# Kernel tuning notes

Measured on AMD Instinct MI355X. Metric: run time of the kernel, lower is better.

## Reference

```python
import jax, jax.numpy as jnp
import numpy as np

N, F, E, WID, M, K = 100000, 128, 128, 4, 25000, 16
HID = WID * F    # width * num_features = 512
DHID = WID * E   # discriminator hidden = 512
EPS = 1e-5


def _v2v(x, v_idx, w_e):
    """Hypergraph v2v mean aggregation: v->e mean (scaled by w_e), then e->v mean."""
    Mm, Kk = v_idx.shape
    C = x.shape[1]
    ef = jnp.zeros((Mm, C), x.dtype)
    for k in range(Kk):  # K is small and static; avoids a [M,K,C] materialization
        ef = ef + x[v_idx[:, k]]
    ef = ef * (w_e / Kk)[:, None]  # weighted edge features [M, C]
    out = jnp.zeros_like(x)
    deg = jnp.zeros((x.shape[0],), x.dtype)
    for k in range(Kk):
        out = out.at[v_idx[:, k]].add(ef)
        deg = deg.at[v_idx[:, k]].add(1.0)
    return out / jnp.maximum(deg, 1.0)[:, None]


def _bn(h, g, bt):
    # BatchNorm1d in training mode: biased batch stats over vertex dim
    m = h.mean(0)
    v = ((h - m) ** 2).mean(0)
    return g * (h - m) * jax.lax.rsqrt(v + EPS) + bt


def _conv(x, Wt, b, g, bt, v_idx, w_e, last=False):
    h = _bn(x @ Wt.T + b, g, bt)
    h = _v2v(h, v_idx, w_e)
    return h if last else jax.nn.relu(h)  # dropout = identity (eval mode)


def setup_inputs() -> dict:
    key = jax.random.key(0)
    ks = iter(jax.random.split(key, 64))

    def lin(o, i):
        s = 1.0 / np.sqrt(i)
        return (jax.random.uniform(next(ks), (o, i), minval=-s, maxval=s, dtype=jnp.float32),
                jax.random.uniform(next(ks), (o,), minval=-s, maxval=s, dtype=jnp.float32))

    d = {}
    d["X"] = jax.random.normal(next(ks), (N, F), dtype=jnp.float32)
    d["v_idx"] = jax.random.randint(next(ks), (M, K), 0, N, dtype=jnp.int32)
    d["w_e"] = jax.random.uniform(next(ks), (M,), dtype=jnp.float32)
    for name, (o, i) in [("enc1", (HID, F)), ("enc2", (E, HID)), ("fc", (E, HID)),
                         ("f1u", (E, E)), ("f2u", (E, E)), ("f1r", (E, E)), ("f2r", (E, E)),
                         ("f1", (E, E)), ("f2", (E, E)),
                         ("dis1", (DHID, E)), ("dis2", (2, DHID)),
                         ("dec1", (HID, E)), ("dec2", (F, HID))]:
        Wt, b = lin(o, i)
        d[name + "_W"] = Wt
        d[name + "_b"] = b
    for name, c in [("enc1", HID), ("enc2", E), ("dis1", DHID), ("dis2", 2), ("dec1", HID), ("dec2", F)]:
        d[name + "_g"] = jnp.ones((c,), jnp.float32)
        d[name + "_bt"] = jnp.zeros((c,), jnp.float32)
    return d


def reference(X, v_idx, w_e,
              enc1_W, enc1_b, enc2_W, enc2_b, fc_W, fc_b,
              f1u_W, f1u_b, f2u_W, f2u_b, f1r_W, f1r_b, f2r_W, f2r_b,
              f1_W, f1_b, f2_W, f2_b,
              dis1_W, dis1_b, dis2_W, dis2_b, dec1_W, dec1_b, dec2_W, dec2_b,
              enc1_g, enc1_bt, enc2_g, enc2_bt, dis1_g, dis1_bt, dis2_g, dis2_bt,
              dec1_g, dec1_bt, dec2_g, dec2_bt):
    # encoder (returns last output and first-layer output)
    x1 = _conv(X, enc1_W, enc1_b, enc1_g, enc1_bt, v_idx, w_e)            # [N, HID]
    xe = _conv(x1, enc2_W, enc2_b, enc2_g, enc2_bt, v_idx, w_e, last=True)  # [N, E]
    xe1 = x1 @ fc_W.T + fc_b                                               # [N, E]
    # GRU-style gating
    z = jax.nn.sigmoid(xe1 @ f1u_W.T + f1u_b + xe @ f2u_W.T + f2u_b)
    r = jax.nn.sigmoid(xe1 @ f1r_W.T + f1r_b + xe @ f2r_W.T + f2r_b)
    o = jnp.tanh(xe1 @ f1_W.T + f1_b + (r * xe) @ f2_W.T + f2_b)
    outs = z * o + (1.0 - z) * xe                                          # [N, E]
    # attention pooling (n = input_size - 1)
    dd = (outs - outs.mean(0)) ** 2
    vv = dd.sum(0) / (N - 1)
    ee = dd / (4.0 * (vv + 0.001)) + 0.5
    proto = (outs * jax.nn.sigmoid(ee)).sum(0)                             # [E]
    # gradient reversal is identity in the forward pass
    h = _conv(outs, dis1_W, dis1_b, dis1_g, dis1_bt, v_idx, w_e)
    xdis = _conv(h, dis2_W, dis2_b, dis2_g, dis2_bt, v_idx, w_e, last=True)  # [N, 2]
    h = _conv(outs, dec1_W, dec1_b, dec1_g, dec1_bt, v_idx, w_e)
    x_de = _conv(h, dec2_W, dec2_b, dec2_g, dec2_bt, v_idx, w_e, last=True)  # [N, F]
    return (outs, x_de, proto, xdis)
```

## Files before the change

kernel.cpp:

```cpp
#include <hip/hip_runtime.h>
#include <cstddef>
#include <cstdint>

static constexpr int NV = 100000;
static constexpr int NP = 100096;
static constexpr int ME = 25000;
static constexpr int MEP = 25088;
static constexpr int KE = 16;
static constexpr float BN_EPS = 1e-5f;

typedef unsigned int u32;
typedef __attribute__((ext_vector_type(8))) short s16x8;
typedef __attribute__((ext_vector_type(8))) unsigned short u16x8;
typedef __attribute__((ext_vector_type(4))) float f32x4;

__device__ __forceinline__ float sigm(float x) { return 1.0f / (1.0f + expf(-x)); }
__device__ __forceinline__ float bf2f(unsigned short u) {
    union { u32 i; float f; } v; v.i = ((u32)u) << 16; return v.f;
}
__device__ __forceinline__ unsigned short f2bf(float f) {
    union { float f; u32 i; } v; v.f = f;
    u32 u = v.i;
    return (unsigned short)((u + 0x7FFFu + ((u >> 16) & 1u)) >> 16);
}

#define GLD16(g, l) __builtin_amdgcn_global_load_lds(                          \
    (__attribute__((address_space(1))) const unsigned int*)(g),                \
    (__attribute__((address_space(3))) unsigned int*)(l), 16, 0, 0)

#define STAGE_AB(b, k0)                                                        \
  {                                                                            \
    unsigned short* sA_ = sm + (b) * 12288;                                    \
    unsigned short* sB_ = sA_ + 8192;                                          \
    _Pragma("unroll")                                                          \
    for (int i_ = 0; i_ < 4; ++i_) {                                           \
      const unsigned short* g_ = A + (size_t)(bm + 32 * w + 8 * i_ + (l >> 3)) * IC + (k0) + swz; \
      GLD16(g_, sA_ + 2048 * w + 512 * i_);                                    \
    }                                                                          \
    _Pragma("unroll")                                                          \
    for (int i_ = 0; i_ < 2; ++i_) {                                           \
      const unsigned short* g_ = W + (size_t)(bn + 16 * w + 8 * i_ + (l >> 3)) * IC + (k0) + swz; \
      GLD16(g_, sB_ + 1024 * w + 512 * i_);                                    \
    }                                                                          \
  }

__global__ __launch_bounds__(256)
void mfma_gemm(const unsigned short* __restrict__ A, int IC,
               const unsigned short* __restrict__ W, const float* __restrict__ bias,
               unsigned short* __restrict__ Cb, int ldb, int cb0,
               unsigned short* __restrict__ Cb2, int ldb2, int splitN,
               float* __restrict__ s1f, float* __restrict__ s2f, int statsC)
{
    __shared__ unsigned short sm[2 * 12288];
    const int bm = blockIdx.y * 128;
    const int bn = blockIdx.x * 64;
    const int tid = threadIdx.x;
    const int l = tid & 63, w = tid >> 6;
    const int wrow = w >> 1, wcol = w & 1;

    f32x4 acc[4][2];
    #pragma unroll
    for (int m = 0; m < 4; ++m)
        #pragma unroll
        for (int n = 0; n < 2; ++n)
            #pragma unroll
            for (int r = 0; r < 4; ++r) acc[m][n][r] = 0.f;

    const int swz = (((l & 7) ^ (l >> 3)) << 3);
    const int nt = IC >> 6;

    STAGE_AB(0, 0);
    asm volatile("s_waitcnt vmcnt(0)" ::: "memory");
    __builtin_amdgcn_s_barrier();

    for (int t = 0; t < nt; ++t) {
        const int cur = t & 1;
        if (t + 1 < nt) STAGE_AB(cur ^ 1, (t + 1) << 6);
        const unsigned short* sA = sm + cur * 12288;
        const unsigned short* sB = sA + 8192;
        #pragma unroll
        for (int ks = 0; ks < 2; ++ks) {
            const int koff = ks * 32 + ((l >> 4) << 3);
            s16x8 afr[4], bfr[2];
            #pragma unroll
            for (int m = 0; m < 4; ++m) {
                int row = wrow * 64 + m * 16 + (l & 15);
                afr[m] = *(const s16x8*)&sA[row * 64 + (koff ^ ((l & 7) << 3))];
            }
            #pragma unroll
            for (int n = 0; n < 2; ++n) {
                int col = wcol * 32 + n * 16 + (l & 15);
                bfr[n] = *(const s16x8*)&sB[col * 64 + (koff ^ ((l & 7) << 3))];
            }
            #pragma unroll
            for (int m = 0; m < 4; ++m)
                #pragma unroll
                for (int n = 0; n < 2; ++n)
                    acc[m][n] = __builtin_amdgcn_mfma_f32_16x16x32_bf16(
                        afr[m], bfr[n], acc[m][n], 0, 0, 0);
        }
        asm volatile("s_waitcnt vmcnt(0)" ::: "memory");
        __builtin_amdgcn_s_barrier();
    }

    unsigned short* dst = Cb;
    int ld = ldb, co = cb0;
    if (Cb2 && bn >= splitN) { dst = Cb2; ld = ldb2; co = -splitN; }

    #pragma unroll
    for (int n = 0; n < 2; ++n) {
        const int col = bn + wcol * 32 + n * 16 + (l & 15);
        const float bs = bias[col];
        float ssum = 0.f, sq = 0.f;
        #pragma unroll
        for (int m = 0; m < 4; ++m) {
            const int row0 = bm + wrow * 64 + m * 16 + ((l >> 4) << 2);
            #pragma unroll
            for (int r = 0; r < 4; ++r) {
                float v = acc[m][n][r] + bs;
                int row = row0 + r;
                if (dst) dst[(size_t)row * ld + co + col] = f2bf(v);
                if (s1f && col < statsC && row < NV) { ssum += v; sq += v * v; }
            }
        }
        if (s1f && col < statsC) {
            ssum += __shfl_xor(ssum, 16); ssum += __shfl_xor(ssum, 32);
            sq   += __shfl_xor(sq, 16);   sq   += __shfl_xor(sq, 32);
            if ((l >> 4) == 0) {
                atomicAdd(&s1f[col], ssum);
                atomicAdd(&s2f[col], sq);
            }
        }
    }
}

__global__ __launch_bounds__(256)
void mfma_gemm_ef(const unsigned short* __restrict__ A,
                  const unsigned short* __restrict__ W,
                  const float* __restrict__ we,
                  const float* __restrict__ P, const float* __restrict__ Q,
                  unsigned short* __restrict__ ef, int ldE)
{
    const int IC = 128;
    __shared__ unsigned short sm[2 * 12288];
    const int bm = blockIdx.y * 128;
    const int bn = blockIdx.x * 64;
    const int tid = threadIdx.x;
    const int l = tid & 63, w = tid >> 6;
    const int wrow = w >> 1, wcol = w & 1;

    f32x4 acc[4][2];
    #pragma unroll
    for (int m = 0; m < 4; ++m)
        #pragma unroll
        for (int n = 0; n < 2; ++n)
            #pragma unroll
            for (int r = 0; r < 4; ++r) acc[m][n][r] = 0.f;

    const int swz = (((l & 7) ^ (l >> 3)) << 3);

    STAGE_AB(0, 0);
    asm volatile("s_waitcnt vmcnt(0)" ::: "memory");
    __builtin_amdgcn_s_barrier();

    #pragma unroll
    for (int t = 0; t < 2; ++t) {
        const int cur = t & 1;
        if (t == 0) STAGE_AB(1, 64);
        const unsigned short* sA = sm + cur * 12288;
        const unsigned short* sB = sA + 8192;
        #pragma unroll
        for (int ks = 0; ks < 2; ++ks) {
            const int koff = ks * 32 + ((l >> 4) << 3);
            s16x8 afr[4], bfr[2];
            #pragma unroll
            for (int m = 0; m < 4; ++m) {
                int row = wrow * 64 + m * 16 + (l & 15);
                afr[m] = *(const s16x8*)&sA[row * 64 + (koff ^ ((l & 7) << 3))];
            }
            #pragma unroll
            for (int n = 0; n < 2; ++n) {
                int col = wcol * 32 + n * 16 + (l & 15);
                bfr[n] = *(const s16x8*)&sB[col * 64 + (koff ^ ((l & 7) << 3))];
            }
            #pragma unroll
            for (int m = 0; m < 4; ++m)
                #pragma unroll
                for (int n = 0; n < 2; ++n)
                    acc[m][n] = __builtin_amdgcn_mfma_f32_16x16x32_bf16(
                        afr[m], bfr[n], acc[m][n], 0, 0, 0);
        }
        asm volatile("s_waitcnt vmcnt(0)" ::: "memory");
        __builtin_amdgcn_s_barrier();
    }

    #pragma unroll
    for (int n = 0; n < 2; ++n) {
        const int col = bn + wcol * 32 + n * 16 + (l & 15);
        const float pc = P[col], qc = Q[col];
        #pragma unroll
        for (int m = 0; m < 4; ++m) {
            const int row0 = bm + wrow * 64 + m * 16 + ((l >> 4) << 2);
            #pragma unroll
            for (int r = 0; r < 4; ++r) {
                int row = row0 + r;
                if (row < ME) {
                    float wv = we[row];
                    ef[(size_t)row * ldE + col] = f2bf(wv * (pc * acc[m][n][r] + qc));
                }
            }
        }
    }
}

__global__ __launch_bounds__(256)
void cov_kernel(const unsigned short* __restrict__ A, float* __restrict__ cov)
{
    __shared__ unsigned short T[128 * 64];
    const int tid = threadIdx.x;
    const int l = tid & 63, w = tid >> 6;

    f32x4 acc[2][8];
    #pragma unroll
    for (int m = 0; m < 2; ++m)
        #pragma unroll
        for (int n = 0; n < 8; ++n)
            #pragma unroll
            for (int r = 0; r < 4; ++r) acc[m][n][r] = 0.f;

    const int r0 = blockIdx.x * 1024;
    for (int ch = 0; ch < 16; ++ch) {
        const int rbase = r0 + ch * 64;
        __syncthreads();
        #pragma unroll
        for (int q = 0; q < 4; ++q) {
            int idx = tid + q * 256;
            int r = idx & 63, cg = idx >> 6;
            int row = rbase + r;
            u16x8 u = {0, 0, 0, 0, 0, 0, 0, 0};
            if (row < NV) u = *(const u16x8*)&A[(size_t)row * 128 + cg * 8];
            #pragma unroll
            for (int j = 0; j < 8; ++j) {
                int c = cg * 8 + j;
                T[c * 64 + (r ^ ((c & 7) << 3))] = u[j];
            }
        }
        __syncthreads();
        #pragma unroll
        for (int ks = 0; ks < 2; ++ks) {
            const int koff = ks * 32 + ((l >> 4) << 3);
            s16x8 fi[2], fj[8];
            #pragma unroll
            for (int m = 0; m < 2; ++m) {
                int c = (w * 2 + m) * 16 + (l & 15);
                fi[m] = *(const s16x8*)&T[c * 64 + (koff ^ ((c & 7) << 3))];
            }
            #pragma unroll
            for (int n = 0; n < 8; ++n) {
                int c = n * 16 + (l & 15);
                fj[n] = *(const s16x8*)&T[c * 64 + (koff ^ ((c & 7) << 3))];
            }
// ... 84 lines not shown
    } else if (i < 492800) {
        int o = i - 492544;
        bzr[o] = (o < 128) ? (f1ub[o] + f2ub[o]) : (f1rb[o - 128] + f2rb[o - 128]);
    } else if (i < 492928) {
        int o = i - 492800;
        bo[o] = f1b[o] + f2b[o];
    } else if (i < 493952) {
        int o = i - 492928;
        bdd[o] = (o < 512) ? ds1b[o] : dc1b[o - 512];
    } else if (i < 494208) {
        int o = i - 493952;
        bef[o] = (o < 128) ? e2b[o] : fcb[o - 128];
    }
}

__global__ void cvt_f32_bf16(const float* __restrict__ in, unsigned short* __restrict__ out, int n)
{
    int i = (blockIdx.x * 256 + threadIdx.x) * 4;
    if (i < n) {
        float4 v = *reinterpret_cast<const float4*>(&in[i]);
        out[i] = f2bf(v.x); out[i + 1] = f2bf(v.y);
        out[i + 2] = f2bf(v.z); out[i + 3] = f2bf(v.w);
    }
}

__global__ void bn_finalize_kernel(const float* __restrict__ s1, const float* __restrict__ s2,
                                   const float* __restrict__ g, const float* __restrict__ bt,
                                   float* __restrict__ scale, float* __restrict__ shift,
                                   int C, float invN)
{
    int c = threadIdx.x;
    if (c < C) {
        float m = s1[c] * invN;
        float v = fmaxf(s2[c] * invN - m * m, 0.f);
        float sc = g[c] * rsqrtf(v + BN_EPS);
        scale[c] = sc;
        shift[c] = bt[c] - m * sc;
    }
}

__global__ void bn_finalize_pq(const float* __restrict__ s1, const float* __restrict__ s2,
                               const float* __restrict__ g, const float* __restrict__ bt,
                               const float* __restrict__ bias,
                               float* __restrict__ P, float* __restrict__ Q,
                               int C, int off, float invN)
{
    int c = threadIdx.x;
    if (c < C) {
        int cc = off + c;
        float m = s1[cc] * invN;
        float v = fmaxf(s2[cc] * invN - m * m, 0.f);
        float sc = g[c] * rsqrtf(v + BN_EPS);
        float sh = bt[c] - m * sc;
        P[cc] = sc * (1.0f / KE);
        Q[cc] = sc * bias[c] + sh;
    }
}

__global__ __launch_bounds__(256)
void edge_gather_sum(const unsigned short* __restrict__ x, const int* __restrict__ vidx,
                     unsigned short* __restrict__ ge)
{
    const int e = blockIdx.x * 16 + (threadIdx.x >> 4);
    const int cp = (threadIdx.x & 15) << 3;
    if (e >= ME) return;
    float s[8] = {};
    const int* vi = vidx + e * KE;
    #pragma unroll
    for (int k = 0; k < KE; ++k) {
        int v = vi[k];
        u16x8 u = *(const u16x8*)&x[(size_t)v * 128 + cp];
        #pragma unroll
        for (int j = 0; j < 8; ++j) s[j] += bf2f(u[j]);
    }
    u16x8 o;
    #pragma unroll
    for (int j = 0; j < 8; ++j) o[j] = f2bf(s[j]);
    *(u16x8*)&ge[(size_t)e * 128 + cp] = o;
}

__global__ __launch_bounds__(256)
void edge_gather_bf(const unsigned short* __restrict__ pre, const int* __restrict__ vidx,
                    const float* __restrict__ we, const float* __restrict__ scl,
                    const float* __restrict__ shf, unsigned short* __restrict__ ef, int C)
{
    const int tpe = C >> 3;
    const int epb = 256 / tpe;
    const int e = blockIdx.x * epb + threadIdx.x / tpe;
    const int cp = (threadIdx.x % tpe) << 3;
    if (e >= ME) return;
    float s[8] = {};
    const int* vi = vidx + e * KE;
    #pragma unroll
    for (int k = 0; k < KE; ++k) {
        int v = vi[k];
        u16x8 u = *(const u16x8*)&pre[(size_t)v * C + cp];
        #pragma unroll
        for (int j = 0; j < 8; ++j) s[j] += bf2f(u[j]);
    }
    float wv = we[e] * (1.0f / KE);
    u16x8 o;
    #pragma unroll
    for (int j = 0; j < 8; ++j)
        o[j] = f2bf(wv * (scl[cp + j] * s[j] + (float)KE * shf[cp + j]));
    *(u16x8*)&ef[(size_t)e * C + cp] = o;
}

__global__ void edge_gather2_kernel(const float* __restrict__ X, const int* __restrict__ vidx,
                                    const float* __restrict__ we, const float* __restrict__ scale,
                                    const float* __restrict__ shift, float* __restrict__ ef)
{
    int e = blockIdx.x * blockDim.x + threadIdx.x;
    if (e >= ME) return;
    float s0 = 0.f, s1v = 0.f;
    #pragma unroll
    for (int k = 0; k < KE; ++k) {
        int v = vidx[e * KE + k];
        s0 += X[2 * v];
        s1v += X[2 * v + 1];
    }
    float w = we[e] * (1.0f / KE);
    ef[2 * e]     = w * (scale[0] * s0 + (float)KE * shift[0]);
    ef[2 * e + 1] = w * (scale[1] * s1v + (float)KE * shift[1]);
}

__global__ void deg_kernel(const int* __restrict__ vidx, int* __restrict__ deg)
{
    int i = blockIdx.x * blockDim.x + threadIdx.x;
    if (i < ME * KE) atomicAdd(&deg[vidx[i]], 1);
}

// ... 51 lines not shown

__global__ __launch_bounds__(256)
void csr_gather_bf(const unsigned short* __restrict__ ef, int ldE, int cb0E,
                   const int* __restrict__ rowptr, const int* __restrict__ csr,
                   float* __restrict__ outf, int ldf,
                   unsigned short* __restrict__ outb, int ldb, int cb0,
                   unsigned short* __restrict__ outb2, int ldb2,
                   int C, int relu)
{
    const int lpv = C >> 3;
    const int vpb = 256 / lpv;
    const int v = blockIdx.x * vpb + threadIdx.x / lpv;
    const int lg = threadIdx.x % lpv;
    if (v >= NV) return;
    const int s = rowptr[v], e = rowptr[v + 1];
    float a[8] = {};
    int i = s;
    for (; i + 2 <= e; i += 2) {
        int e0 = csr[i], e1 = csr[i + 1];
        u16x8 u0 = *(const u16x8*)&ef[(size_t)e0 * ldE + cb0E + lg * 8];
        u16x8 u1 = *(const u16x8*)&ef[(size_t)e1 * ldE + cb0E + lg * 8];
        #pragma unroll
        for (int j = 0; j < 8; ++j) a[j] += bf2f(u0[j]) + bf2f(u1[j]);
    }
    if (i < e) {
        int e0 = csr[i];
        u16x8 u0 = *(const u16x8*)&ef[(size_t)e0 * ldE + cb0E + lg * 8];
        #pragma unroll
        for (int j = 0; j < 8; ++j) a[j] += bf2f(u0[j]);
    }
    float inv = 1.0f / (float)max(e - s, 1);
    #pragma unroll
    for (int j = 0; j < 8; ++j) {
        float x = a[j] * inv;
        if (relu) x = fmaxf(x, 0.f);
        a[j] = x;
    }
    if (outf) {
        float* p = outf + (size_t)v * ldf + lg * 8;
        #pragma unroll
        for (int j = 0; j < 8; ++j) p[j] = a[j];
    }
    if (outb) {
        u16x8 o;
        #pragma unroll
        for (int j = 0; j < 8; ++j) o[j] = f2bf(a[j]);
        *(u16x8*)&outb[(size_t)v * ldb + cb0 + lg * 8] = o;
    }
    if (outb2) {
        u16x8 o;
        #pragma unroll
        for (int j = 0; j < 8; ++j) o[j] = f2bf(a[j]);
        *(u16x8*)&outb2[(size_t)v * ldb2 + lg * 8] = o;
    }
}

__global__ __launch_bounds__(256)
void csr_gather_dd(const unsigned short* __restrict__ ef,
                   const int* __restrict__ rowptr, const int* __restrict__ csr,
                   const unsigned short* __restrict__ wdis2, const float* __restrict__ dis2b,
                   float* __restrict__ pre22, unsigned short* __restrict__ hdec)
{
    const int w = threadIdx.x >> 6, l = threadIdx.x & 63;
    const int v = blockIdx.x * 2 + (w >> 1);
    const int half = w & 1;
    const int s = rowptr[v], e = rowptr[v + 1];
    const int cp = half * 512 + l * 8;
    float a[8] = {};
    int i = s;
    for (; i + 2 <= e; i += 2) {
        int e0 = csr[i], e1 = csr[i + 1];
        u16x8 u0 = *(const u16x8*)&ef[(size_t)e0 * 1024 + cp];
        u16x8 u1 = *(const u16x8*)&ef[(size_t)e1 * 1024 + cp];
        #pragma unroll
        for (int j = 0; j < 8; ++j) a[j] += bf2f(u0[j]) + bf2f(u1[j]);
    }
    if (i < e) {
        int e0 = csr[i];
        u16x8 u0 = *(const u16x8*)&ef[(size_t)e0 * 1024 + cp];
        #pragma unroll
        for (int j = 0; j < 8; ++j) a[j] += bf2f(u0[j]);
    }
    float inv = 1.0f / (float)max(e - s, 1);
    #pragma unroll
    for (int j = 0; j < 8; ++j) a[j] = fmaxf(a[j] * inv, 0.f);
    if (half == 0) {
        u16x8 w0 = *(const u16x8*)&wdis2[l * 8];
        u16x8 w1 = *(const u16x8*)&wdis2[512 + l * 8];
        float d0 = 0.f, d1 = 0.f;
        #pragma unroll
        for (int j = 0; j < 8; ++j) {
            d0 += a[j] * bf2f(w0[j]);
            d1 += a[j] * bf2f(w1[j]);
        }
        for (int o = 32; o > 0; o >>= 1) {
            d0 += __shfl_down(d0, o);
            d1 += __shfl_down(d1, o);
        }
        if (l == 0) {
            pre22[2 * v]     = d0 + dis2b[0];
            pre22[2 * v + 1] = d1 + dis2b[1];
        }
    } else {
        u16x8 o8;
        #pragma unroll
        for (int j = 0; j < 8; ++j) o8[j] = f2bf(a[j]);
        *(u16x8*)&hdec[(size_t)v * 512 + l * 8] = o8;
    }
}

__global__ void csr_gather2_kernel(const float* __restrict__ ef, const int* __restrict__ rowptr,
                                   const int* __restrict__ csr, float* __restrict__ outp)
{
    int v = blockIdx.x * blockDim.x + threadIdx.x;
    if (v >= NV) return;
    int s = rowptr[v], e = rowptr[v + 1];
    float a0 = 0.f, a1 = 0.f;
    for (int i = s; i < e; ++i) {
        int ed = csr[i];
        a0 += ef[2 * ed];
        a1 += ef[2 * ed + 1];
    }
    float inv = 1.0f / (float)max(e - s, 1);
    outp[2 * v]     = a0 * inv;
    outp[2 * v + 1] = a1 * inv;
}

__global__ __launch_bounds__(256)
void colstats_bf(const unsigned short* __restrict__ Xb,
                 float* __restrict__ s1, float* __restrict__ s2)
{
    const int t = threadIdx.x;
    const int cg = t & 15;
    const int rs = t >> 4;
    float s[8] = {}, q[8] = {};
    for (int r = blockIdx.x * 16 + rs; r < NV; r += 256 * 16) {
        u16x8 u = *(const u16x8*)&Xb[(size_t)r * 128 + cg * 8];
        #pragma unroll
        for (int j = 0; j < 8; ++j) {
            float v = bf2f(u[j]);
            s[j] += v; q[j] += v * v;
        }
    }
    __shared__ float ls[16][16][8];
    __shared__ float lq[16][16][8];
    #pragma unroll
    for (int j = 0; j < 8; ++j) { ls[rs][cg][j] = s[j]; lq[rs][cg][j] = q[j]; }
    __syncthreads();
    int c = t & 127;
    float a = 0.f;
    if (t < 128) {
        #pragma unroll
        for (int i = 0; i < 16; ++i) a += ls[i][c >> 3][c & 7];
        atomicAdd(&s1[c], a);
    } else {
        #pragma unroll
        for (int i = 0; i < 16; ++i) a += lq[i][c >> 3][c & 7];
        atomicAdd(&s2[c], a);
    }
}
// ... 130 lines not shown
    const float* f1u_W  = (const float*)d_in[9];  const float* f1u_b  = (const float*)d_in[10];
    const float* f2u_W  = (const float*)d_in[11]; const float* f2u_b  = (const float*)d_in[12];
    const float* f1r_W  = (const float*)d_in[13]; const float* f1r_b  = (const float*)d_in[14];
    const float* f2r_W  = (const float*)d_in[15]; const float* f2r_b  = (const float*)d_in[16];
    const float* f1_W   = (const float*)d_in[17]; const float* f1_b   = (const float*)d_in[18];
    const float* f2_W   = (const float*)d_in[19]; const float* f2_b   = (const float*)d_in[20];
    const float* dis1_W = (const float*)d_in[21]; const float* dis1_b = (const float*)d_in[22];
    const float* dis2_W = (const float*)d_in[23]; const float* dis2_b = (const float*)d_in[24];
    const float* dec1_W = (const float*)d_in[25]; const float* dec1_b = (const float*)d_in[26];
    const float* dec2_W = (const float*)d_in[27]; const float* dec2_b = (const float*)d_in[28];
    const float* enc1_g = (const float*)d_in[29]; const float* enc1_bt = (const float*)d_in[30];
    const float* enc2_g = (const float*)d_in[31]; const float* enc2_bt = (const float*)d_in[32];
    const float* dis1_g = (const float*)d_in[33]; const float* dis1_bt = (const float*)d_in[34];
    const float* dis2_g = (const float*)d_in[35]; const float* dis2_bt = (const float*)d_in[36];
    const float* dec1_g = (const float*)d_in[37]; const float* dec1_bt = (const float*)d_in[38];
    const float* dec2_g = (const float*)d_in[39]; const float* dec2_bt = (const float*)d_in[40];

    float* out   = (float*)d_out;
    float* outs  = out;
    float* x_de  = out + 12800000;
    float* proto = out + 25600000;
    float* xdis  = out + 25600128;

    char* base = (char*)d_ws;
    unsigned short* bufA = (unsigned short*)base;
    char* p = base + (size_t)NP * 512 * 2;
    unsigned short* bufE = (unsigned short*)p; p += (size_t)MEP * 1024 * 2;
    unsigned short* Greg = (unsigned short*)p;
    unsigned short* Xbf  = Greg;
    unsigned short* outsb = Greg + (size_t)NP * 128;
    p += (size_t)NP * 256 * 2;
    unsigned short* x1bf = (unsigned short*)p; p += (size_t)NP * 512 * 2;
    unsigned short* WB = (unsigned short*)p; p += 492544 * 2 + 1024;
    float* bzr = (float*)p; p += 256 * 4;
    float* bo  = (float*)p; p += 128 * 4;
    float* bdd = (float*)p; p += 1024 * 4;
    float* bef = (float*)p; p += 256 * 4;
    float* s1  = (float*)p; p += 1024 * 4;
    float* s2  = (float*)p; p += 1024 * 4;
    float* scl = (float*)p; p += 1024 * 4;
    float* shf = (float*)p; p += 1024 * 4;
    float* sX1 = (float*)p; p += 128 * 4;
    float* sX2 = (float*)p; p += 128 * 4;
    float* sA1 = (float*)p; p += 128 * 4;
    float* sA2 = (float*)p; p += 128 * 4;
    float* covX = (float*)p; p += 16384 * 4;
    float* covA = (float*)p; p += 16384 * 4;
    int* deg    = (int*)p; p += (size_t)NV * 4;
    int* rowptr = (int*)p; p += (size_t)(NV + 1) * 4;
    int* cursor = (int*)p; p += (size_t)NV * 4;
    int* bsums  = (int*)p; p += 512 * 4;
    int* csr    = (int*)p; p += (size_t)ME * KE * 4;
    float* outsf = (float*)p; p += (size_t)NP * 128 * 4;
    unsigned short* ge = (unsigned short*)p;

    unsigned short* pre128 = bufA;
    unsigned short* xe_bf  = bufA + (size_t)NP * 128;
    unsigned short* ZR     = bufA + (size_t)NP * 256;
    unsigned short* Opre   = bufA;
    unsigned short* hdec   = bufA;
    float* pre22 = (float*)(Greg + (size_t)NP * 128);
    float* bufEf = (float*)bufE;

    unsigned short* wenc1 = WB;
    unsigned short* wenc2 = WB + 65536;
    unsigned short* wdd   = WB + 196608;
    unsigned short* wdec2 = WB + 327680;
    unsigned short* wdis2 = WB + 393216;
    unsigned short* wzr   = WB + 394240;
    unsigned short* wo    = WB + 459776;

    const int n128 = NV * 128;
    const int n8 = n128 / 8;
    const int nScanBlocks = (NV + 255) / 256;

    auto gemm = [&](const unsigned short* A, int ic, const unsigned short* W, const float* b,
                    unsigned short* Cb, int ldb, int cb0,
                    unsigned short* Cb2, int ldb2, int splitN,
                    int oc, float* st1, float* st2, int statsC) {
        dim3 g(oc / 64, NP / 128);
        mfma_gemm<<<g, 256, 0, stream>>>(A, ic, W, b, Cb, ldb, cb0, Cb2, ldb2, splitN,
                                         st1, st2, statsC);
    };

    prep_weights<<<1931, 256, 0, stream>>>(enc1_W, enc2_W, fc_W, dis1_W, dec1_W, dec2_W, dis2_W,
                                           f1u_W, f2u_W, f1r_W, f2r_W, f1_W, f2_W,
                                           f1u_b, f2u_b, f1r_b, f2r_b, f1_b, f2_b,
                                           dis1_b, dec1_b, enc2_b, fc_b,
                                           WB, bzr, bo, bdd, bef);
    cvt_f32_bf16<<<(n128 / 4 + 255) / 256, 256, 0, stream>>>(X, Xbf, n128);

    hipMemsetAsync(deg, 0, NV * sizeof(int), stream);
    deg_kernel<<<(ME * KE + 255) / 256, 256, 0, stream>>>(vidx, deg);
    scan_block_kernel<<<nScanBlocks, 256, 0, stream>>>(deg, rowptr, bsums, NV);
    scan_sums_par<<<1, 512, 0, stream>>>(bsums, nScanBlocks);
    scan_add_kernel<<<nScanBlocks, 256, 0, stream>>>(rowptr, bsums, NV);
    hipMemcpyAsync(cursor, rowptr, NV * sizeof(int), hipMemcpyDeviceToDevice, stream);
    csr_fill_kernel<<<(ME * KE + 255) / 256, 256, 0, stream>>>(vidx, cursor, csr);

    hipMemsetAsync(sX1, 0, 256 * sizeof(float), stream);
    hipMemsetAsync(covX, 0, 16384 * sizeof(float), stream);
    colstats_bf<<<256, 256, 0, stream>>>(Xbf, sX1, sX2);
    cov_kernel<<<98, 256, 0, stream>>>(Xbf, covX);
    quadform_kernel<<<512, 128, 0, stream>>>(covX, sX1, wenc1, enc1_b, s1, s2);
    bn_finalize_pq<<<1, 512, 0, stream>>>(s1, s2, enc1_g, enc1_bt, enc1_b, scl, shf, 512, 0, 1.0f / NV);
    edge_gather_sum<<<(ME + 15) / 16, 256, 0, stream>>>(Xbf, vidx, ge);
    { dim3 g(8, MEP / 128);
      mfma_gemm_ef<<<g, 256, 0, stream>>>(ge, wenc1, we, scl, shf, bufE, 512); }
    csr_gather_bf<<<NV / 4, 256, 0, stream>>>(bufE, 512, 0, rowptr, csr,
        nullptr, 0, x1bf, 512, 0, nullptr, 0, 512, 1);

    hipMemsetAsync(s1, 0, 2048 * sizeof(float), stream);
    gemm(x1bf, 512, wenc2, bef, pre128, 128, 0, Greg, 256, 128, 256, s1, s2, 128);
    bn_finalize_kernel<<<1, 512, 0, stream>>>(s1, s2, enc2_g, enc2_bt, scl, shf, 128, 1.0f / NV);
    edge_gather_bf<<<(ME + 15) / 16, 256, 0, stream>>>(pre128, vidx, we, scl, shf, bufE, 128);
    csr_gather_bf<<<NV / 16, 256, 0, stream>>>(bufE, 128, 0, rowptr, csr,
        nullptr, 0, Greg, 256, 128, xe_bf, 128, 128, 0);

    gemm(Greg, 256, wzr, bzr, ZR, 256, 0, nullptr, 0, 1 << 30, 256, nullptr, nullptr, 0);
    rx_kernel<<<(n8 + 255) / 256, 256, 0, stream>>>(ZR, xe_bf, Greg, n8);
    gemm(Greg, 256, wo, bo, Opre, 128, 0, nullptr, 0, 1 << 30, 128, nullptr, nullptr, 0);
    gru_out_kernel<<<(n8 + 255) / 256, 256, 0, stream>>>(ZR, Opre, xe_bf, outs, outsb, outsf, n8);

    hipMemsetAsync(sA1, 0, 256 * sizeof(float), stream);
    colstats_bf<<<256, 256, 0, stream>>>(outsb, sA1, sA2);
    att_finalize_kernel<<<1, 128, 0, stream>>>(sA1, sA2, scl, shf, 128);
    hipMemsetAsync(proto, 0, 128 * sizeof(float), stream);
    proto_ws<<<256, 256, 0, stream>>>(outsf, scl, shf, proto);

    hipMemsetAsync(covA, 0, 16384 * sizeof(float), stream);
    cov_kernel<<<98, 256, 0, stream>>>(outsb, covA);
    quadform_kernel<<<1024, 128, 0, stream>>>(covA, sA1, wdd, bdd, s1, s2);
    bn_finalize_pq<<<1, 512, 0, stream>>>(s1, s2, dis1_g, dis1_bt, dis1_b, scl, shf, 512, 0, 1.0f / NV);
    bn_finalize_pq<<<1, 512, 0, stream>>>(s1, s2, dec1_g, dec1_bt, dec1_b, scl, shf, 512, 512, 1.0f / NV);
    edge_gather_sum<<<(ME + 15) / 16, 256, 0, stream>>>(outsb, vidx, ge);
    { dim3 g(16, MEP / 128);
      mfma_gemm_ef<<<g, 256, 0, stream>>>(ge, wdd, we, scl, shf, bufE, 1024); }
    csr_gather_dd<<<NV / 2, 256, 0, stream>>>(bufE, rowptr, csr, wdis2, dis2_b, pre22, hdec);

    hipMemsetAsync(s1, 0, 2048 * sizeof(float), stream);
    colstats2_kernel<<<64, 256, 0, stream>>>(pre22, NV, s1, s2);
    bn_finalize_kernel<<<1, 512, 0, stream>>>(s1, s2, dis2_g, dis2_bt, scl, shf, 2, 1.0f / NV);
    edge_gather2_kernel<<<(ME + 255) / 256, 256, 0, stream>>>(pre22, vidx, we, scl, shf, bufEf);
    csr_gather2_kernel<<<(NV + 255) / 256, 256, 0, stream>>>(bufEf, rowptr, csr, xdis);

    hipMemsetAsync(s1, 0, 2048 * sizeof(float), stream);
    gemm(hdec, 512, wdec2, dec2_b, Greg, 128, 0, nullptr, 0, 1 << 30, 128, s1, s2, 128);
    bn_finalize_kernel<<<1, 512, 0, stream>>>(s1, s2, dec2_g, dec2_bt, scl, shf, 128, 1.0f / NV);
    edge_gather_bf<<<(ME + 15) / 16, 256, 0, stream>>>(Greg, vidx, we, scl, shf, bufE, 128);
    csr_gather_bf<<<NV / 16, 256, 0, stream>>>(bufE, 128, 0, rowptr, csr,
        x_de, 128, nullptr, 0, 0, nullptr, 0, 128, 0);
}
```

Measured before the change: 901.1 us.

## Reorder v2v aggregation before the linear layer to gather narrow inputs

Uses linearity of BN-affine plus mean aggregation to move the weighted edge-to-vertex gather onto the 128-wide input features. Each vertex gets a weighted sum of incident edge sums and a mean edge weight, and the 512/1024-wide GEMM then runs on the vertex rows with ReLU and the BN scale/shift applied in its epilogue. This removes the wide per-edge output buffer and the wide CSR gather over it. The dis2 projection is folded into the GEMM epilogue through shuffle reductions and atomics into pre22. In exchange the GEMM covers four times as many rows, bf16 rounding happens at a different point, and the dis2 bias is dropped because the following batch norm cancels it.

```diff
diff --git a/kernel.cpp b/kernel.cpp
--- a/kernel.cpp
+++ b/kernel.cpp
@@ -135,11 +135,13 @@
 }
 
 __global__ __launch_bounds__(256)
-void mfma_gemm_ef(const unsigned short* __restrict__ A,
-                  const unsigned short* __restrict__ W,
-                  const float* __restrict__ we,
-                  const float* __restrict__ P, const float* __restrict__ Q,
-                  unsigned short* __restrict__ ef, int ldE)
+void mfma_gemm_vtx(const unsigned short* __restrict__ A,
+                   const unsigned short* __restrict__ W,
+                   const float* __restrict__ P, const float* __restrict__ Q,
+                   const float* __restrict__ sw,
+                   unsigned short* __restrict__ dst, int ldd, int colStart,
+                   const unsigned short* __restrict__ disW,
+                   float* __restrict__ pre22)
 {
     const int IC = 128;
     __shared__ unsigned short sm[2 * 12288];
@@ -194,19 +196,44 @@
         __builtin_amdgcn_s_barrier();
     }
 
-    #pragma unroll
-    for (int n = 0; n < 2; ++n) {
-        const int col = bn + wcol * 32 + n * 16 + (l & 15);
-        const float pc = P[col], qc = Q[col];
+    if (disW && bn < colStart) {
         #pragma unroll
         for (int m = 0; m < 4; ++m) {
-            const int row0 = bm + wrow * 64 + m * 16 + ((l >> 4) << 2);
             #pragma unroll
             for (int r = 0; r < 4; ++r) {
-                int row = row0 + r;
-                if (row < ME) {
-                    float wv = we[row];
-                    ef[(size_t)row * ldE + col] = f2bf(wv * (pc * acc[m][n][r] + qc));
+                const int row = bm + wrow * 64 + m * 16 + ((l >> 4) << 2) + r;
+                const float swr = sw[row];
+                float p0 = 0.f, p1 = 0.f;
+                #pragma unroll
+                for (int n = 0; n < 2; ++n) {
+                    const int col = bn + wcol * 32 + n * 16 + (l & 15);
+                    float h = fmaxf(P[col] * acc[m][n][r] + swr * Q[col], 0.f);
+                    p0 += h * bf2f(disW[col]);
+                    p1 += h * bf2f(disW[512 + col]);
+                }
+                p0 += __shfl_xor(p0, 1); p0 += __shfl_xor(p0, 2);
+                p0 += __shfl_xor(p0, 4); p0 += __shfl_xor(p0, 8);
+                p1 += __shfl_xor(p1, 1); p1 += __shfl_xor(p1, 2);
+                p1 += __shfl_xor(p1, 4); p1 += __shfl_xor(p1, 8);
+                if ((l & 15) == 0 && row < NV) {
+                    atomicAdd(&pre22[2 * row], p0);
+                    atomicAdd(&pre22[2 * row + 1], p1);
+                }
+            }
+        }
+    } else {
+        #pragma unroll
+        for (int n = 0; n < 2; ++n) {
+            const int col = bn + wcol * 32 + n * 16 + (l & 15);
+            const float pc = P[col], qc = Q[col];
+            #pragma unroll
+            for (int m = 0; m < 4; ++m) {
+                const int row0 = bm + wrow * 64 + m * 16 + ((l >> 4) << 2);
+                #pragma unroll
+                for (int r = 0; r < 4; ++r) {
+                    const int row = row0 + r;
+                    float h = fmaxf(pc * acc[m][n][r] + sw[row] * qc, 0.f);
+                    dst[(size_t)row * ldd + col - colStart] = f2bf(h);
                 }
             }
         }
@@ -397,7 +424,7 @@
         float v = fmaxf(s2[cc] * invN - m * m, 0.f);
         float sc = g[c] * rsqrtf(v + BN_EPS);
         float sh = bt[c] - m * sc;
-        P[cc] = sc * (1.0f / KE);
+        P[cc] = sc;
         Q[cc] = sc * bias[c] + sh;
     }
 }
@@ -422,6 +449,40 @@
     #pragma unroll
     for (int j = 0; j < 8; ++j) o[j] = f2bf(s[j]);
     *(u16x8*)&ge[(size_t)e * 128 + cp] = o;
+}
+
+__global__ __launch_bounds__(256)
+void csr_gather_g2(const unsigned short* __restrict__ ge, const float* __restrict__ we,
+                   const int* __restrict__ rowptr, const int* __restrict__ csr,
+                   unsigned short* __restrict__ g2, float* __restrict__ swv)
+{
+    const int v = blockIdx.x * 16 + (threadIdx.x >> 4);
+    const int lg = threadIdx.x & 15;
+    if (v >= NP) return;
+    if (v >= NV) {
+        u16x8 z = {0, 0, 0, 0, 0, 0, 0, 0};
+        *(u16x8*)&g2[(size_t)v * 128 + lg * 8] = z;
+        if (swv && lg == 0) swv[v] = 0.f;
+        return;
+    }
+    const int s = rowptr[v], e = rowptr[v + 1];
+    float a[8] = {};
+    float ws = 0.f;
+    for (int i = s; i < e; ++i) {
+        int ed = csr[i];
+        float wt = we[ed];
+        ws += wt;
+        u16x8 u = *(const u16x8*)&ge[(size_t)ed * 128 + lg * 8];
+        #pragma unroll
+        for (int j = 0; j < 8; ++j) a[j] = fmaf(wt, bf2f(u[j]), a[j]);
+    }
+    float inv = 1.0f / (float)max(e - s, 1);
+    float invK = inv * (1.0f / KE);
+    u16x8 o;
+    #pragma unroll
+    for (int j = 0; j < 8; ++j) o[j] = f2bf(a[j] * invK);
+    *(u16x8*)&g2[(size_t)v * 128 + lg * 8] = o;
+    if (swv && lg == 0) swv[v] = ws * inv;
 }
 
 __global__ __launch_bounds__(256)
@@ -579,60 +640,6 @@
         #pragma unroll
         for (int j = 0; j < 8; ++j) o[j] = f2bf(a[j]);
         *(u16x8*)&outb2[(size_t)v * ldb2 + lg * 8] = o;
-    }
-}
-
-__global__ __launch_bounds__(256)
-void csr_gather_dd(const unsigned short* __restrict__ ef,
-                   const int* __restrict__ rowptr, const int* __restrict__ csr,
-                   const unsigned short* __restrict__ wdis2, const float* __restrict__ dis2b,
-                   float* __restrict__ pre22, unsigned short* __restrict__ hdec)
-{
-    const int w = threadIdx.x >> 6, l = threadIdx.x & 63;
-    const int v = blockIdx.x * 2 + (w >> 1);
-    const int half = w & 1;
-    const int s = rowptr[v], e = rowptr[v + 1];
-    const int cp = half * 512 + l * 8;
-    float a[8] = {};
-    int i = s;
-    for (; i + 2 <= e; i += 2) {
-        int e0 = csr[i], e1 = csr[i + 1];
-        u16x8 u0 = *(const u16x8*)&ef[(size_t)e0 * 1024 + cp];
-        u16x8 u1 = *(const u16x8*)&ef[(size_t)e1 * 1024 + cp];
-        #pragma unroll
-        for (int j = 0; j < 8; ++j) a[j] += bf2f(u0[j]) + bf2f(u1[j]);
-    }
-    if (i < e) {
-        int e0 = csr[i];
-        u16x8 u0 = *(const u16x8*)&ef[(size_t)e0 * 1024 + cp];
-        #pragma unroll
-        for (int j = 0; j < 8; ++j) a[j] += bf2f(u0[j]);
-    }
-    float inv = 1.0f / (float)max(e - s, 1);
-    #pragma unroll
-    for (int j = 0; j < 8; ++j) a[j] = fmaxf(a[j] * inv, 0.f);
-    if (half == 0) {
-        u16x8 w0 = *(const u16x8*)&wdis2[l * 8];
-        u16x8 w1 = *(const u16x8*)&wdis2[512 + l * 8];
-        float d0 = 0.f, d1 = 0.f;
-        #pragma unroll
-        for (int j = 0; j < 8; ++j) {
-            d0 += a[j] * bf2f(w0[j]);
-            d1 += a[j] * bf2f(w1[j]);
-        }
-        for (int o = 32; o > 0; o >>= 1) {
-            d0 += __shfl_down(d0, o);
-            d1 += __shfl_down(d1, o);
-        }
-        if (l == 0) {
-            pre22[2 * v]     = d0 + dis2b[0];
-            pre22[2 * v + 1] = d1 + dis2b[1];
-        }
-    } else {
-        u16x8 o8;
-        #pragma unroll
-        for (int j = 0; j < 8; ++j) o8[j] = f2bf(a[j]);
-        *(u16x8*)&hdec[(size_t)v * 512 + l * 8] = o8;
     }
 }
 
@@ -869,7 +876,10 @@
     int* bsums  = (int*)p; p += 512 * 4;
     int* csr    = (int*)p; p += (size_t)ME * KE * 4;
     float* outsf = (float*)p; p += (size_t)NP * 128 * 4;
-    unsigned short* ge = (unsigned short*)p;
+    unsigned short* ge = (unsigned short*)p; p += (size_t)MEP * 128 * 2;
+    float* sw = (float*)p;
+
+    unsigned short* g2 = bufE + (size_t)MEP * 128;
 
     unsigned short* pre128 = bufA;
     unsigned short* xe_bf  = bufA + (size_t)NP * 128;
@@ -922,10 +932,10 @@
     quadform_kernel<<<512, 128, 0, stream>>>(covX, sX1, wenc1, enc1_b, s1, s2);
     bn_finalize_pq<<<1, 512, 0, stream>>>(s1, s2, enc1_g, enc1_bt, enc1_b, scl, shf, 512, 0, 1.0f / NV);
     edge_gather_sum<<<(ME + 15) / 16, 256, 0, stream>>>(Xbf, vidx, ge);
-    { dim3 g(8, MEP / 128);
-      mfma_gemm_ef<<<g, 256, 0, stream>>>(ge, wenc1, we, scl, shf, bufE, 512); }
-    csr_gather_bf<<<NV / 4, 256, 0, stream>>>(bufE, 512, 0, rowptr, csr,
-        nullptr, 0, x1bf, 512, 0, nullptr, 0, 512, 1);
+    csr_gather_g2<<<NP / 16, 256, 0, stream>>>(ge, we, rowptr, csr, g2, sw);
+    { dim3 g(8, NP / 128);
+      mfma_gemm_vtx<<<g, 256, 0, stream>>>(g2, wenc1, scl, shf, sw, x1bf, 512, 0,
+                                           nullptr, nullptr); }
 
     hipMemsetAsync(s1, 0, 2048 * sizeof(float), stream);
     gemm(x1bf, 512, wenc2, bef, pre128, 128, 0, Greg, 256, 128, 256, s1, s2, 128);
@@ -951,9 +961,11 @@
     bn_finalize_pq<<<1, 512, 0, stream>>>(s1, s2, dis1_g, dis1_bt, dis1_b, scl, shf, 512, 0, 1.0f / NV);
     bn_finalize_pq<<<1, 512, 0, stream>>>(s1, s2, dec1_g, dec1_bt, dec1_b, scl, shf, 512, 512, 1.0f / NV);
     edge_gather_sum<<<(ME + 15) / 16, 256, 0, stream>>>(outsb, vidx, ge);
-    { dim3 g(16, MEP / 128);
-      mfma_gemm_ef<<<g, 256, 0, stream>>>(ge, wdd, we, scl, shf, bufE, 1024); }
-    csr_gather_dd<<<NV / 2, 256, 0, stream>>>(bufE, rowptr, csr, wdis2, dis2_b, pre22, hdec);
+    csr_gather_g2<<<NP / 16, 256, 0, stream>>>(ge, we, rowptr, csr, g2, nullptr);
+    hipMemsetAsync(pre22, 0, (size_t)NV * 2 * sizeof(float), stream);
+    { dim3 g(16, NP / 128);
+      mfma_gemm_vtx<<<g, 256, 0, stream>>>(g2, wdd, scl, shf, sw, hdec, 512, 512,
+                                           wdis2, pre22); }
 
     hipMemsetAsync(s1, 0, 2048 * sizeof(float), stream);
     colstats2_kernel<<<64, 256, 0, stream>>>(pre22, NV, s1, s2);
```

After: 938.8 us. +4.2%, slower.

## Read GEMM B operand directly from global and split dis/dec edge buffers

Applied to the files above, without the earlier changes.

The GEMM kernels stop staging the weight (B) tile in shared memory and load B fragments straight from global memory, which cuts LDS use per block and may raise occupancy. This relies on the small weight matrix hitting in cache but adds uncoalesced global loads inside the MFMA loop. The edge-feature GEMM now writes the dis and dec halves into two separate 512-wide buffers. The fused 1024-wide csr gather is replaced by a dis-only gather kernel plus the generic bf16 gather for the dec half. Each gather reads contiguous 512-wide rows, at the cost of an extra launch and a second traversal of the CSR.

```diff
diff --git a/kernel.cpp b/kernel.cpp
--- a/kernel.cpp
+++ b/kernel.cpp
@@ -28,19 +28,13 @@
     (__attribute__((address_space(1))) const unsigned int*)(g),                \
     (__attribute__((address_space(3))) unsigned int*)(l), 16, 0, 0)
 
-#define STAGE_AB(b, k0)                                                        \
+#define STAGE_A(b, k0)                                                         \
   {                                                                            \
-    unsigned short* sA_ = sm + (b) * 12288;                                    \
-    unsigned short* sB_ = sA_ + 8192;                                          \
+    unsigned short* sA_ = sm + (b) * 8192;                                     \
     _Pragma("unroll")                                                          \
     for (int i_ = 0; i_ < 4; ++i_) {                                           \
       const unsigned short* g_ = A + (size_t)(bm + 32 * w + 8 * i_ + (l >> 3)) * IC + (k0) + swz; \
       GLD16(g_, sA_ + 2048 * w + 512 * i_);                                    \
-    }                                                                          \
-    _Pragma("unroll")                                                          \
-    for (int i_ = 0; i_ < 2; ++i_) {                                           \
-      const unsigned short* g_ = W + (size_t)(bn + 16 * w + 8 * i_ + (l >> 3)) * IC + (k0) + swz; \
-      GLD16(g_, sB_ + 1024 * w + 512 * i_);                                    \
     }                                                                          \
   }
 
@@ -51,7 +45,7 @@
                unsigned short* __restrict__ Cb2, int ldb2, int splitN,
                float* __restrict__ s1f, float* __restrict__ s2f, int statsC)
 {
-    __shared__ unsigned short sm[2 * 12288];
+    __shared__ unsigned short sm[2 * 8192];
     const int bm = blockIdx.y * 128;
     const int bn = blockIdx.x * 64;
     const int tid = threadIdx.x;
@@ -69,15 +63,14 @@
     const int swz = (((l & 7) ^ (l >> 3)) << 3);
     const int nt = IC >> 6;
 
-    STAGE_AB(0, 0);
+    STAGE_A(0, 0);
     asm volatile("s_waitcnt vmcnt(0)" ::: "memory");
     __builtin_amdgcn_s_barrier();
 
     for (int t = 0; t < nt; ++t) {
         const int cur = t & 1;
-        if (t + 1 < nt) STAGE_AB(cur ^ 1, (t + 1) << 6);
-        const unsigned short* sA = sm + cur * 12288;
-        const unsigned short* sB = sA + 8192;
+        if (t + 1 < nt) STAGE_A(cur ^ 1, (t + 1) << 6);
+        const unsigned short* sA = sm + cur * 8192;
         #pragma unroll
         for (int ks = 0; ks < 2; ++ks) {
             const int koff = ks * 32 + ((l >> 4) << 3);
@@ -89,8 +82,8 @@
             }
             #pragma unroll
             for (int n = 0; n < 2; ++n) {
-                int col = wcol * 32 + n * 16 + (l & 15);
-                bfr[n] = *(const s16x8*)&sB[col * 64 + (koff ^ ((l & 7) << 3))];
+                int col = bn + wcol * 32 + n * 16 + (l & 15);
+                bfr[n] = *(const s16x8*)&W[(size_t)col * IC + (t << 6) + koff];
             }
             #pragma unroll
             for (int m = 0; m < 4; ++m)
@@ -135,14 +128,14 @@
 }
 
 __global__ __launch_bounds__(256)
-void mfma_gemm_ef(const unsigned short* __restrict__ A,
-                  const unsigned short* __restrict__ W,
-                  const float* __restrict__ we,
-                  const float* __restrict__ P, const float* __restrict__ Q,
-                  unsigned short* __restrict__ ef, int ldE)
+void mfma_gemm_ef2(const unsigned short* __restrict__ A,
+                   const unsigned short* __restrict__ W,
+                   const float* __restrict__ we,
+                   const float* __restrict__ P, const float* __restrict__ Q,
+                   unsigned short* __restrict__ ef0, unsigned short* __restrict__ ef1)
 {
     const int IC = 128;
-    __shared__ unsigned short sm[2 * 12288];
+    __shared__ unsigned short sm[2 * 8192];
     const int bm = blockIdx.y * 128;
     const int bn = blockIdx.x * 64;
     const int tid = threadIdx.x;
@@ -159,16 +152,15 @@
 
     const int swz = (((l & 7) ^ (l >> 3)) << 3);
 
-    STAGE_AB(0, 0);
+    STAGE_A(0, 0);
     asm volatile("s_waitcnt vmcnt(0)" ::: "memory");
     __builtin_amdgcn_s_barrier();
 
     #pragma unroll
     for (int t = 0; t < 2; ++t) {
         const int cur = t & 1;
-        if (t == 0) STAGE_AB(1, 64);
-        const unsigned short* sA = sm + cur * 12288;
-        const unsigned short* sB = sA + 8192;
+        if (t == 0) STAGE_A(1, 64);
+        const unsigned short* sA = sm + cur * 8192;
         #pragma unroll
         for (int ks = 0; ks < 2; ++ks) {
             const int koff = ks * 32 + ((l >> 4) << 3);
@@ -180,8 +172,8 @@
             }
             #pragma unroll
             for (int n = 0; n < 2; ++n) {
-                int col = wcol * 32 + n * 16 + (l & 15);
-                bfr[n] = *(const s16x8*)&sB[col * 64 + (koff ^ ((l & 7) << 3))];
+                int col = bn + wcol * 32 + n * 16 + (l & 15);
+                bfr[n] = *(const s16x8*)&W[(size_t)col * 128 + (t << 6) + koff];
             }
             #pragma unroll
             for (int m = 0; m < 4; ++m)
@@ -194,10 +186,13 @@
         __builtin_amdgcn_s_barrier();
     }
 
+    unsigned short* dst = (bn < 512) ? ef0 : ef1;
+    const int co = (bn < 512) ? 0 : -512;
+
     #pragma unroll
     for (int n = 0; n < 2; ++n) {
-        const int col = bn + wcol * 32 + n * 16 + (l & 15);
-        const float pc = P[col], qc = Q[col];
+        const int colg = bn + wcol * 32 + n * 16 + (l & 15);
+        const float pc = P[colg], qc = Q[colg];
         #pragma unroll
         for (int m = 0; m < 4; ++m) {
             const int row0 = bm + wrow * 64 + m * 16 + ((l >> 4) << 2);
@@ -206,7 +201,7 @@
                 int row = row0 + r;
                 if (row < ME) {
                     float wv = we[row];
-                    ef[(size_t)row * ldE + col] = f2bf(wv * (pc * acc[m][n][r] + qc));
+                    dst[(size_t)row * 512 + co + colg] = f2bf(wv * (pc * acc[m][n][r] + qc));
                 }
             }
         }
@@ -583,56 +578,47 @@
 }
 
 __global__ __launch_bounds__(256)
-void csr_gather_dd(const unsigned short* __restrict__ ef,
-                   const int* __restrict__ rowptr, const int* __restrict__ csr,
-                   const unsigned short* __restrict__ wdis2, const float* __restrict__ dis2b,
-                   float* __restrict__ pre22, unsigned short* __restrict__ hdec)
+void csr_gather_dis(const unsigned short* __restrict__ ef,
+                    const int* __restrict__ rowptr, const int* __restrict__ csr,
+                    const unsigned short* __restrict__ wdis2, const float* __restrict__ dis2b,
+                    float* __restrict__ pre22)
 {
     const int w = threadIdx.x >> 6, l = threadIdx.x & 63;
-    const int v = blockIdx.x * 2 + (w >> 1);
-    const int half = w & 1;
+    const int v = blockIdx.x * 4 + w;
+    if (v >= NV) return;
     const int s = rowptr[v], e = rowptr[v + 1];
-    const int cp = half * 512 + l * 8;
     float a[8] = {};
     int i = s;
     for (; i + 2 <= e; i += 2) {
         int e0 = csr[i], e1 = csr[i + 1];
-        u16x8 u0 = *(const u16x8*)&ef[(size_t)e0 * 1024 + cp];
-        u16x8 u1 = *(const u16x8*)&ef[(size_t)e1 * 1024 + cp];
+        u16x8 u0 = *(const u16x8*)&ef[(size_t)e0 * 512 + l * 8];
+        u16x8 u1 = *(const u16x8*)&ef[(size_t)e1 * 512 + l * 8];
         #pragma unroll
         for (int j = 0; j < 8; ++j) a[j] += bf2f(u0[j]) + bf2f(u1[j]);
     }
     if (i < e) {
         int e0 = csr[i];
-        u16x8 u0 = *(const u16x8*)&ef[(size_t)e0 * 1024 + cp];
+        u16x8 u0 = *(const u16x8*)&ef[(size_t)e0 * 512 + l * 8];
         #pragma unroll
         for (int j = 0; j < 8; ++j) a[j] += bf2f(u0[j]);
     }
     float inv = 1.0f / (float)max(e - s, 1);
-    #pragma unroll
-    for (int j = 0; j < 8; ++j) a[j] = fmaxf(a[j] * inv, 0.f);
-    if (half == 0) {
-        u16x8 w0 = *(const u16x8*)&wdis2[l * 8];
-        u16x8 w1 = *(const u16x8*)&wdis2[512 + l * 8];
-        float d0 = 0.f, d1 = 0.f;
-        #pragma unroll
-        for (int j = 0; j < 8; ++j) {
-            d0 += a[j] * bf2f(w0[j]);
-            d1 += a[j] * bf2f(w1[j]);
-        }
-        for (int o = 32; o > 0; o >>= 1) {
-            d0 += __shfl_down(d0, o);
-            d1 += __shfl_down(d1, o);
-        }
-        if (l == 0) {
-            pre22[2 * v]     = d0 + dis2b[0];
-            pre22[2 * v + 1] = d1 + dis2b[1];
-        }
-    } else {
-        u16x8 o8;
-        #pragma unroll
-        for (int j = 0; j < 8; ++j) o8[j] = f2bf(a[j]);
-        *(u16x8*)&hdec[(size_t)v * 512 + l * 8] = o8;
+    u16x8 w0 = *(const u16x8*)&wdis2[l * 8];
+    u16x8 w1 = *(const u16x8*)&wdis2[512 + l * 8];
+    float d0 = 0.f, d1 = 0.f;
+    #pragma unroll
+    for (int j = 0; j < 8; ++j) {
+        float h = fmaxf(a[j] * inv, 0.f);
+        d0 += h * bf2f(w0[j]);
+        d1 += h * bf2f(w1[j]);
+    }
+    for (int o = 32; o > 0; o >>= 1) {
+        d0 += __shfl_down(d0, o);
+        d1 += __shfl_down(d1, o);
+    }
+    if (l == 0) {
+        pre22[2 * v]     = d0 + dis2b[0];
+        pre22[2 * v + 1] = d1 + dis2b[1];
     }
 }
 
@@ -871,6 +857,9 @@
     float* outsf = (float*)p; p += (size_t)NP * 128 * 4;
     unsigned short* ge = (unsigned short*)p;
 
+    unsigned short* bufE0 = bufE;
+    unsigned short* bufE1 = bufE + (size_t)MEP * 512;
+
     unsigned short* pre128 = bufA;
     unsigned short* xe_bf  = bufA + (size_t)NP * 128;
     unsigned short* ZR     = bufA + (size_t)NP * 256;
@@ -923,15 +912,15 @@
     bn_finalize_pq<<<1, 512, 0, stream>>>(s1, s2, enc1_g, enc1_bt, enc1_b, scl, shf, 512, 0, 1.0f / NV);
     edge_gather_sum<<<(ME + 15) / 16, 256, 0, stream>>>(Xbf, vidx, ge);
     { dim3 g(8, MEP / 128);
-      mfma_gemm_ef<<<g, 256, 0, stream>>>(ge, wenc1, we, scl, shf, bufE, 512); }
-    csr_gather_bf<<<NV / 4, 256, 0, stream>>>(bufE, 512, 0, rowptr, csr,
+      mfma_gemm_ef2<<<g, 256, 0, stream>>>(ge, wenc1, we, scl, shf, bufE0, bufE1); }
+    csr_gather_bf<<<NV / 4, 256, 0, stream>>>(bufE0, 512, 0, rowptr, csr,
         nullptr, 0, x1bf, 512, 0, nullptr, 0, 512, 1);
 
     hipMemsetAsync(s1, 0, 2048 * sizeof(float), stream);
     gemm(x1bf, 512, wenc2, bef, pre128, 128, 0, Greg, 256, 128, 256, s1, s2, 128);
     bn_finalize_kernel<<<1, 512, 0, stream>>>(s1, s2, enc2_g, enc2_bt, scl, shf, 128, 1.0f / NV);
-    edge_gather_bf<<<(ME + 15) / 16, 256, 0, stream>>>(pre128, vidx, we, scl, shf, bufE, 128);
-    csr_gather_bf<<<NV / 16, 256, 0, stream>>>(bufE, 128, 0, rowptr, csr,
+    edge_gather_bf<<<(ME + 15) / 16, 256, 0, stream>>>(pre128, vidx, we, scl, shf, bufE0, 128);
+    csr_gather_bf<<<NV / 16, 256, 0, stream>>>(bufE0, 128, 0, rowptr, csr,
         nullptr, 0, Greg, 256, 128, xe_bf, 128, 128, 0);
 
     gemm(Greg, 256, wzr, bzr, ZR, 256, 0, nullptr, 0, 1 << 30, 256, nullptr, nullptr, 0);
@@ -952,8 +941,10 @@
     bn_finalize_pq<<<1, 512, 0, stream>>>(s1, s2, dec1_g, dec1_bt, dec1_b, scl, shf, 512, 512, 1.0f / NV);
     edge_gather_sum<<<(ME + 15) / 16, 256, 0, stream>>>(outsb, vidx, ge);
     { dim3 g(16, MEP / 128);
-      mfma_gemm_ef<<<g, 256, 0, stream>>>(ge, wdd, we, scl, shf, bufE, 1024); }
-    csr_gather_dd<<<NV / 2, 256, 0, stream>>>(bufE, rowptr, csr, wdis2, dis2_b, pre22, hdec);
+      mfma_gemm_ef2<<<g, 256, 0, stream>>>(ge, wdd, we, scl, shf, bufE0, bufE1); }
+    csr_gather_dis<<<NV / 4, 256, 0, stream>>>(bufE0, rowptr, csr, wdis2, dis2_b, pre22);
+    csr_gather_bf<<<NV / 4, 256, 0, stream>>>(bufE1, 512, 0, rowptr, csr,
+        nullptr, 0, hdec, 512, 0, nullptr, 0, 512, 1);
 
     hipMemsetAsync(s1, 0, 2048 * sizeof(float), stream);
     colstats2_kernel<<<64, 256, 0, stream>>>(pre22, NV, s1, s2);
@@ -964,7 +955,7 @@
     hipMemsetAsync(s1, 0, 2048 * sizeof(float), stream);
     gemm(hdec, 512, wdec2, dec2_b, Greg, 128, 0, nullptr, 0, 1 << 30, 128, s1, s2, 128);
     bn_finalize_kernel<<<1, 512, 0, stream>>>(s1, s2, dec2_g, dec2_bt, scl, shf, 128, 1.0f / NV);
-    edge_gather_bf<<<(ME + 15) / 16, 256, 0, stream>>>(Greg, vidx, we, scl, shf, bufE, 128);
-    csr_gather_bf<<<NV / 16, 256, 0, stream>>>(bufE, 128, 0, rowptr, csr,
+    edge_gather_bf<<<(ME + 15) / 16, 256, 0, stream>>>(Greg, vidx, we, scl, shf, bufE0, 128);
+    csr_gather_bf<<<NV / 16, 256, 0, stream>>>(bufE0, 128, 0, rowptr, csr,
         x_de, 128, nullptr, 0, 0, nullptr, 0, 128, 0);
 }
```

Result: no change. 910.8 us (+1.1%).
